# Performance work log

Hardware: AMD Instinct MI355X
Metric: run time of the kernel (lower is better)

## Reference

```python
import jax, jax.numpy as jnp
import numpy as np

HIDDEN = 256
HEADS = 8
HEAD_DIM = HIDDEN // HEADS
N = 4096
EPS = 1e-5


def setup_inputs() -> dict:
    key = jax.random.key(0)
    ks = jax.random.split(key, 16)
    s = HIDDEN ** -0.5
    inp = {
        "A": jax.random.uniform(ks[0], (N, N), dtype=jnp.float32),
        "h": jax.random.normal(ks[1], (N, HIDDEN), dtype=jnp.float32),
        # Linear layers stored torch-style as [out, in]
        "Wq": jax.random.normal(ks[2], (HIDDEN, HIDDEN), jnp.float32) * s,
        "bq": jnp.zeros((HIDDEN,), jnp.float32),
        "Wk": jax.random.normal(ks[3], (HIDDEN, HIDDEN), jnp.float32) * s,
        "bk": jnp.zeros((HIDDEN,), jnp.float32),
        "Wv": jax.random.normal(ks[4], (HIDDEN, HIDDEN), jnp.float32) * s,
        "bv": jnp.zeros((HIDDEN,), jnp.float32),
        "Wo": jax.random.normal(ks[5], (HIDDEN, HIDDEN), jnp.float32) * s,
        "bo": jnp.zeros((HIDDEN,), jnp.float32),
        "W1": jax.random.normal(ks[6], (2 * HIDDEN, HIDDEN), jnp.float32) * s,
        "c1": jnp.zeros((2 * HIDDEN,), jnp.float32),
        "W2": jax.random.normal(ks[7], (HIDDEN, 2 * HIDDEN), jnp.float32) * (2 * HIDDEN) ** -0.5,
        "c2": jnp.zeros((HIDDEN,), jnp.float32),
        "g1": jnp.ones((HIDDEN,), jnp.float32),
        "be1": jnp.zeros((HIDDEN,), jnp.float32),
        "g2": jnp.ones((HIDDEN,), jnp.float32),
        "be2": jnp.zeros((HIDDEN,), jnp.float32),
    }
    return inp


def _batchnorm(x, gamma, beta):
    # BatchNorm1d training mode: biased batch stats over node axis
    mean = x.mean(axis=0)
    var = ((x - mean) ** 2).mean(axis=0)
    return (x - mean) * jax.lax.rsqrt(var + EPS) * gamma + beta


def _mha(A, h, Wq, bq, Wk, bk, Wv, bv, Wo, bo):
    n = h.shape[0]
    scaling = HEAD_DIM ** -0.5
    # NOTE: raw reshape [N, H*d] -> (H, N, d), exactly as the torch code (no transpose)
    q = ((h @ Wq.T + bq).reshape(HEADS, n, HEAD_DIM)) * scaling
    k = (h @ Wk.T + bk).reshape(HEADS, n, HEAD_DIM)
    v = (h @ Wv.T + bv).reshape(HEADS, n, HEAD_DIM)
    t = jnp.einsum('hnd,hmd->hnm', q, k)          # [H, N, N]
    attn = jax.nn.softmax(t * A, axis=2)          # multiplicative adjacency mask
    out = jnp.einsum('hnm,hmd->hnd', attn, v)     # [H, N, d]
    return out.reshape(n, -1) @ Wo.T + bo         # raw reshape back, as in torch


def reference(A, h, Wq, bq, Wk, bk, Wv, bv, Wo, bo, W1, c1, W2, c2, g1, be1, g2, be2):
    h1 = h
    x = _mha(A, h, Wq, bq, Wk, bk, Wv, bv, Wo, bo)
    x = _batchnorm(x + h1, g1, be1)
    h2 = x
    x = jax.nn.relu(x @ W1.T + c1) @ W2.T + c2
    return _batchnorm(h2 + x, g2, be2)
```

## Files before the change

kernel.cpp:

```cpp
#include <hip/hip_runtime.h>

#define N_NODES 4096
#define HID 256
#define NHEADS 8
#define HDIM 32
#define EPSV 1e-5f
#define M2LOG 11.541560327111707f

typedef __bf16 bf16x8 __attribute__((ext_vector_type(8)));
typedef __bf16 bf16x4 __attribute__((ext_vector_type(4)));
typedef float f32x4 __attribute__((ext_vector_type(4)));

__device__ inline float fexp2(float x) {
    float r;
    asm("v_exp_f32 %0, %1" : "=v"(r) : "v"(x));
    return r;
}

__device__ inline uint4 pack8(float4 a, float4 b) {
    bf16x8 p;
    p[0]=(__bf16)a.x; p[1]=(__bf16)a.y; p[2]=(__bf16)a.z; p[3]=(__bf16)a.w;
    p[4]=(__bf16)b.x; p[5]=(__bf16)b.y; p[6]=(__bf16)b.z; p[7]=(__bf16)b.w;
    return __builtin_bit_cast(uint4, p);
}
__device__ inline float4 nmad4(float4 x, float4 s, float4 sh) {
    return make_float4(fmaf(x.x,s.x,sh.x), fmaf(x.y,s.y,sh.y),
                       fmaf(x.z,s.z,sh.z), fmaf(x.w,s.w,sh.w));
}

__launch_bounds__(256)
__global__ void gemm_mfma(const float* __restrict__ X, const float* __restrict__ W,
                          const float* __restrict__ bias, const float* __restrict__ resid,
                          float* __restrict__ C,
                          const float* __restrict__ nscale, const float* __restrict__ nshift,
                          const float* __restrict__ rscale, const float* __restrict__ rshift,
                          int M, int N, int K, float scale, int do_relu) {
    __shared__ uint4 xl[2][512];
    __shared__ uint4 wl[2][512];
    const int bm = blockIdx.x * 64, bn = blockIdx.y * 64;
    const int t = threadIdx.x;
    const int w = t >> 6, l = t & 63, g = l >> 4, nl = l & 15;
    const int srow = t >> 3, seg = t & 7;
    const int sx = (seg & 3) << 1;
    const int d0 = seg*64 + (srow ^ sx);
    const int d1 = seg*64 + ((srow + 32) ^ sx);
    const float* xp = X + (size_t)(bm + srow)*K + seg*8;
    const float* wp = W + (size_t)(bn + srow)*K + seg*8;
    const size_t rstep = (size_t)32*K;

    f32x4 acc[4];
    #pragma unroll
    for (int nf = 0; nf < 4; ++nf) acc[nf] = (f32x4){0.f,0.f,0.f,0.f};

    {
        float4 x0 = *(const float4*)(xp),          x1 = *(const float4*)(xp + 4);
        float4 x2 = *(const float4*)(xp + rstep),  x3 = *(const float4*)(xp + rstep + 4);
        if (nscale) {
            float4 s0 = *(const float4*)(nscale + seg*8), s1 = *(const float4*)(nscale + seg*8 + 4);
            float4 h0 = *(const float4*)(nshift + seg*8), h1 = *(const float4*)(nshift + seg*8 + 4);
            x0 = nmad4(x0,s0,h0); x1 = nmad4(x1,s1,h1);
            x2 = nmad4(x2,s0,h0); x3 = nmad4(x3,s1,h1);
        }
        float4 w0 = *(const float4*)(wp),          w1 = *(const float4*)(wp + 4);
        float4 w2 = *(const float4*)(wp + rstep),  w3 = *(const float4*)(wp + rstep + 4);
        xl[0][d0] = pack8(x0, x1); xl[0][d1] = pack8(x2, x3);
        wl[0][d0] = pack8(w0, w1); wl[0][d1] = pack8(w2, w3);
    }
    __syncthreads();

    for (int k0 = 0; k0 < K; k0 += 64) {
        const int cur = (k0 >> 6) & 1;
        const bool nxt = (k0 + 64) < K;
        float4 nx0, nx1, nx2, nx3, nw0, nw1, nw2, nw3;
        if (nxt) {
            const int kk = k0 + 64;
            nx0 = *(const float4*)(xp + kk);          nx1 = *(const float4*)(xp + kk + 4);
            nx2 = *(const float4*)(xp + rstep + kk);  nx3 = *(const float4*)(xp + rstep + kk + 4);
            if (nscale) {
                float4 s0 = *(const float4*)(nscale + kk + seg*8), s1 = *(const float4*)(nscale + kk + seg*8 + 4);
                float4 h0 = *(const float4*)(nshift + kk + seg*8), h1 = *(const float4*)(nshift + kk + seg*8 + 4);
                nx0 = nmad4(nx0,s0,h0); nx1 = nmad4(nx1,s1,h1);
                nx2 = nmad4(nx2,s0,h0); nx3 = nmad4(nx3,s1,h1);
            }
            nw0 = *(const float4*)(wp + kk);          nw1 = *(const float4*)(wp + kk + 4);
            nw2 = *(const float4*)(wp + rstep + kk);  nw3 = *(const float4*)(wp + rstep + kk + 4);
        }
        __builtin_amdgcn_s_setprio(1);
        #pragma unroll
        for (int ks = 0; ks < 2; ++ks) {
            bf16x8 af = __builtin_bit_cast(bf16x8, xl[cur][(ks*4 + g)*64 + ((w*16 + nl) ^ (g << 1))]);
            #pragma unroll
            for (int nf = 0; nf < 4; ++nf) {
                bf16x8 bfr = __builtin_bit_cast(bf16x8, wl[cur][(ks*4 + g)*64 + ((nf*16 + nl) ^ (g << 1))]);
                acc[nf] = __builtin_amdgcn_mfma_f32_16x16x32_bf16(af, bfr, acc[nf], 0, 0, 0);
            }
        }
        __builtin_amdgcn_s_setprio(0);
        if (nxt) {
            xl[cur^1][d0] = pack8(nx0, nx1); xl[cur^1][d1] = pack8(nx2, nx3);
            wl[cur^1][d0] = pack8(nw0, nw1); wl[cur^1][d1] = pack8(nw2, nw3);
        }
        __syncthreads();
    }

    #pragma unroll
    for (int nf = 0; nf < 4; ++nf) {
        const int col = bn + nf*16 + nl;
        const float bb = bias[col];
        float rs = 1.f, rh = 0.f;
        if (rscale) { rs = rscale[col]; rh = rshift[col]; }
        #pragma unroll
        for (int r = 0; r < 4; ++r) {
            const int row = bm + w*16 + g*4 + r;
            float v = acc[nf][r] + bb;
            if (resid) {
                float rv = resid[(size_t)row*N + col];
                v += rscale ? fmaf(rv, rs, rh) : rv;
            }
            v *= scale;
            if (do_relu) v = fmaxf(v, 0.f);
            C[(size_t)row*N + col] = v;
        }
    }
}

__launch_bounds__(256)
__global__ void gemm_qkv(const float* __restrict__ X,
                         const float* __restrict__ Wq, const float* __restrict__ Wk,
                         const float* __restrict__ Wv, const float* __restrict__ bq,
                         const float* __restrict__ bk, const float* __restrict__ bv,
                         __bf16* __restrict__ qhat, __bf16* __restrict__ khat,
                         __bf16* __restrict__ vhat) {
    const int K = 256;
    __shared__ uint4 xl[2][512];
    __shared__ uint4 wl[2][512];
    const int z = blockIdx.z;
    const float* W = (z == 0) ? Wq : (z == 1) ? Wk : Wv;
    const float* bias = (z == 0) ? bq : (z == 1) ? bk : bv;
    __bf16* hat = (z == 0) ? qhat : (z == 1) ? khat : vhat;
    const float scale = (z == 0) ? 0.25506595325f : 1.f;

    const int bm = blockIdx.x * 64, bn = blockIdx.y * 64;
    const int t = threadIdx.x;
    const int w = t >> 6, l = t & 63, g = l >> 4, nl = l & 15;
    const int srow = t >> 3, seg = t & 7;
    const int sx = (seg & 3) << 1;
    const int d0 = seg*64 + (srow ^ sx);
    const int d1 = seg*64 + ((srow + 32) ^ sx);
    const float* xp = X + (size_t)(bm + srow)*K + seg*8;
    const float* wp = W + (size_t)(bn + srow)*K + seg*8;
    const size_t rstep = (size_t)32*K;

    f32x4 acc[4];
    #pragma unroll
    for (int nf = 0; nf < 4; ++nf) acc[nf] = (f32x4){0.f,0.f,0.f,0.f};

    {
        float4 x0 = *(const float4*)(xp),          x1 = *(const float4*)(xp + 4);
        float4 x2 = *(const float4*)(xp + rstep),  x3 = *(const float4*)(xp + rstep + 4);
        float4 w0 = *(const float4*)(wp),          w1 = *(const float4*)(wp + 4);
        float4 w2 = *(const float4*)(wp + rstep),  w3 = *(const float4*)(wp + rstep + 4);
        xl[0][d0] = pack8(x0, x1); xl[0][d1] = pack8(x2, x3);
        wl[0][d0] = pack8(w0, w1); wl[0][d1] = pack8(w2, w3);
    }
    __syncthreads();

    for (int k0 = 0; k0 < K; k0 += 64) {
        const int cur = (k0 >> 6) & 1;
        const bool nxt = (k0 + 64) < K;
        float4 nx0, nx1, nx2, nx3, nw0, nw1, nw2, nw3;
        if (nxt) {
            nx0 = *(const float4*)(xp + k0 + 64);          nx1 = *(const float4*)(xp + k0 + 68);
            nx2 = *(const float4*)(xp + rstep + k0 + 64);  nx3 = *(const float4*)(xp + rstep + k0 + 68);
            nw0 = *(const float4*)(wp + k0 + 64);          nw1 = *(const float4*)(wp + k0 + 68);
            nw2 = *(const float4*)(wp + rstep + k0 + 64);  nw3 = *(const float4*)(wp + rstep + k0 + 68);
        }
        __builtin_amdgcn_s_setprio(1);
        #pragma unroll
        for (int ks = 0; ks < 2; ++ks) {
            bf16x8 af = __builtin_bit_cast(bf16x8, xl[cur][(ks*4 + g)*64 + ((w*16 + nl) ^ (g << 1))]);
            #pragma unroll
            for (int nf = 0; nf < 4; ++nf) {
                bf16x8 bfr = __builtin_bit_cast(bf16x8, wl[cur][(ks*4 + g)*64 + ((nf*16 + nl) ^ (g << 1))]);
                acc[nf] = __builtin_amdgcn_mfma_f32_16x16x32_bf16(af, bfr, acc[nf], 0, 0, 0);
            }
        }
        __builtin_amdgcn_s_setprio(0);
        if (nxt) {
            xl[cur^1][d0] = pack8(nx0, nx1); xl[cur^1][d1] = pack8(nx2, nx3);
            wl[cur^1][d0] = pack8(nw0, nw1); wl[cur^1][d1] = pack8(nw2, nw3);
        }
        __syncthreads();
    }

    #pragma unroll
    for (int nf = 0; nf < 4; ++nf) {
        const int col = bn + nf*16 + nl;
        const float bb = bias[col];
        #pragma unroll
        for (int r = 0; r < 4; ++r) {
            const int row = bm + w*16 + g*4 + r;
            float v = (acc[nf][r] + bb) * scale;
            const int hh = row >> 9;
            const int nn = ((row & 511) << 3) | (col >> 5);
            hat[((size_t)(hh*4096 + nn))*32 + (col & 31)] = (__bf16)v;
        }
    }
}

__launch_bounds__(256)
__global__ void transpose_vhat(const __bf16* __restrict__ vhat, __bf16* __restrict__ vT) {
    const int h = blockIdx.y, n0 = blockIdx.x * 64;
    __shared__ __bf16 tile[64][40];
    const int t = threadIdx.x;
    {
        int n = t >> 2, dd0 = (t & 3) * 8;
        *(uint4*)&tile[n][dd0] = *(const uint4*)(vhat + ((size_t)(h*4096 + n0 + n))*32 + dd0);
    }
    __syncthreads();
    {
        int d = t >> 3, ns = (t & 7) * 8;
        uint4 ov;
        __bf16* op = (__bf16*)&ov;
        #pragma unroll
        for (int j = 0; j < 8; ++j) op[j] = tile[ns + j][d];
        *(uint4*)(vT + ((size_t)(h*32 + d))*4096 + n0 + ns) = ov;
    }
}

__launch_bounds__(256)
__global__ void attn_mfma(const __bf16* __restrict__ qh, const __bf16* __restrict__ kh,
                          const __bf16* __restrict__ vT, const float* __restrict__ A,
                          float* __restrict__ Opart, float* __restrict__ Lpart, int mlen) {
    __shared__ float A_lds[2][32][76];
    __shared__ uint4 p_lds[4][2][64];

    const int t = threadIdx.x;
    const int w = t >> 6, l = t & 63;
    const int g = l >> 4, nl = l & 15;
    const int h = blockIdx.y * 4 + w;
    const int n0 = blockIdx.x * 32;
    const int z = blockIdx.z;
    const int m_begin = z * mlen;
    const int nsteps = mlen >> 6;

    bf16x8 qf[2];
    #pragma unroll
    for (int nf = 0; nf < 2; ++nf)
        qf[nf] = *(const bf16x8*)(qh + ((size_t)(h*4096 + n0 + nf*16 + nl))*32 + g*8);

    f32x4 oacc[2][2];
    #pragma unroll
    for (int nf = 0; nf < 2; ++nf) {
        oacc[nf][0] = (f32x4){0.f,0.f,0.f,0.f};
        oacc[nf][1] = (f32x4){0.f,0.f,0.f,0.f};
    }
    float Li[2] = {0.f, 0.f};

    const int aq = t >> 3, am = (t & 7) * 8;
    const float* Abase = A + (size_t)(n0 + aq)*N_NODES + m_begin + am;
    const __bf16* kbase = kh + ((size_t)h*4096 + nl)*32 + g*8;
    const __bf16* vbase = vT + ((size_t)h*32 + nl)*4096 + g*8;

    *(float4*)&A_lds[0][aq][am]   = *(const float4*)(Abase);
    *(float4*)&A_lds[0][aq][am+4] = *(const float4*)(Abase + 4);
    bf16x8 kcur[4];
    #pragma unroll
    for (int tt = 0; tt < 4; ++tt)
        kcur[tt] = *(const bf16x8*)(kbase + (size_t)(m_begin + tt*16)*32);
    asm volatile("s_waitcnt lgkmcnt(0)" ::: "memory");
    __builtin_amdgcn_s_barrier();

    for (int s = 0; s < nsteps; ++s) {
        const int cur = s & 1;
        const int m0 = m_begin + s*64;
        const int sn = (s + 1 < nsteps) ? (s + 1) : s;
        const int mn = m_begin + sn*64;

        bf16x8 vcur[4];
        #pragma unroll
        for (int half = 0; half < 2; ++half)
            #pragma unroll
            for (int dt = 0; dt < 2; ++dt)
                vcur[half*2+dt] = *(const bf16x8*)(vbase + (size_t)dt*16*4096 + m0 + half*32);
        float4 a0n = *(const float4*)(Abase + sn*64);
        float4 a1n = *(const float4*)(Abase + sn*64 + 4);
        bf16x8 knx[4];
        #pragma unroll
        for (int tt = 0; tt < 4; ++tt)
            knx[tt] = *(const bf16x8*)(kbase + (size_t)(mn + tt*16)*32);
        __builtin_amdgcn_sched_barrier(0);

        #pragma unroll
        for (int half = 0; half < 2; ++half) {
            #pragma unroll
            for (int tt2 = 0; tt2 < 2; ++tt2) {
                const int tt = half*2 + tt2;
                f32x4 st[2];
                __builtin_amdgcn_s_setprio(1);
                #pragma unroll
                for (int nf = 0; nf < 2; ++nf) {
                    f32x4 zz = (f32x4){0.f,0.f,0.f,0.f};
                    st[nf] = __builtin_amdgcn_mfma_f32_16x16x32_bf16(kcur[tt], qf[nf], zz, 0, 0, 0);
                }
                __builtin_amdgcn_s_setprio(0);
                #pragma unroll
                for (int nf = 0; nf < 2; ++nf) {
                    const f32x4 a4 = *(const f32x4*)&A_lds[cur][nf*16 + nl][tt*16 + g*4];
                    float p0 = fexp2(fmaf(st[nf][0], a4[0], -M2LOG));
                    float p1 = fexp2(fmaf(st[nf][1], a4[1], -M2LOG));
                    float p2 = fexp2(fmaf(st[nf][2], a4[2], -M2LOG));
                    float p3 = fexp2(fmaf(st[nf][3], a4[3], -M2LOG));
                    Li[nf] += (p0 + p1) + (p2 + p3);
                    bf16x4 pk;
                    pk[0] = (__bf16)p0; pk[1] = (__bf16)p1;
                    pk[2] = (__bf16)p2; pk[3] = (__bf16)p3;
                    const int gm = tt2*2 + (g >> 1);
                    *(bf16x4*)((char*)&p_lds[w][nf][0] + (gm*16 + (nl ^ (gm << 1)))*16 + (g & 1)*8) = pk;
                }
            }
            __builtin_amdgcn_s_setprio(1);
            #pragma unroll
            for (int nf = 0; nf < 2; ++nf) {
                bf16x8 pf = __builtin_bit_cast(bf16x8, p_lds[w][nf][g*16 + (nl ^ (g << 1))]);
                #pragma unroll
                for (int dt = 0; dt < 2; ++dt)
                    oacc[nf][dt] = __builtin_amdgcn_mfma_f32_16x16x32_bf16(vcur[half*2+dt], pf, oacc[nf][dt], 0, 0, 0);
            }
            __builtin_amdgcn_s_setprio(0);
        }

        if (s + 1 < nsteps) {
            *(float4*)&A_lds[cur^1][aq][am]   = a0n;
            *(float4*)&A_lds[cur^1][aq][am+4] = a1n;
        }
        #pragma unroll
        for (int tt = 0; tt < 4; ++tt) kcur[tt] = knx[tt];
        asm volatile("s_waitcnt lgkmcnt(0)" ::: "memory");
        __builtin_amdgcn_s_barrier();
    }

    #pragma unroll
    for (int nf = 0; nf < 2; ++nf) {
        Li[nf] += __shfl_xor(Li[nf], 16);
        Li[nf] += __shfl_xor(Li[nf], 32);
        const int nq = n0 + nf*16 + nl;
        float* ob = Opart + ((size_t)(z*NHEADS + h)*4096 + nq)*32;
        #pragma unroll
        for (int dt = 0; dt < 2; ++dt)
            *(float4*)(ob + dt*16 + g*4) = make_float4(oacc[nf][dt][0], oacc[nf][dt][1],
                                                       oacc[nf][dt][2], oacc[nf][dt][3]);
        if (g == 0)
            Lpart[(z*NHEADS + h)*4096 + nq] = Li[nf];
    }
}

__launch_bounds__(256)
__global__ void attn_combine(const float* __restrict__ Opart, const float* __restrict__ Lpart,
                             float* __restrict__ AO, int nsplit) {
    const int idx4 = (blockIdx.x * 256 + threadIdx.x) * 4;
    const int hn = idx4 >> 5;
    float L = 0.f;
    float4 acc = make_float4(0.f, 0.f, 0.f, 0.f);
    for (int zz = 0; zz < nsplit; ++zz) {
        L += Lpart[zz*32768 + hn];
        float4 o = *(const float4*)(Opart + (size_t)zz*1048576 + idx4);
        acc.x += o.x; acc.y += o.y; acc.z += o.z; acc.w += o.w;
    }
    const float inv = 1.f / L;
    *(float4*)(AO + idx4) = make_float4(acc.x*inv, acc.y*inv, acc.z*inv, acc.w*inv);
}

__launch_bounds__(256)
__global__ void colstats_part(const float* __restrict__ X, float* __restrict__ ps,
                              float* __restrict__ pq) {
    const int b = blockIdx.x, t = threadIdx.x;
    float s = 0.f, q = 0.f;
    const float* p = X + (size_t)b*64*HID + t;
    #pragma unroll 8
    for (int r = 0; r < 64; ++r) {
        float v = p[r*HID];
        s += v; q = fmaf(v, v, q);
    }
    ps[b*HID + t] = s;
    pq[b*HID + t] = q;
}

__launch_bounds__(256)
__global__ void colstats_fin(const float* __restrict__ ps, const float* __restrict__ pq,
                             const float* __restrict__ gam, const float* __restrict__ bet,
                             float* __restrict__ scl, float* __restrict__ shf) {
    const int c = threadIdx.x;
    float s = 0.f, q = 0.f;
    #pragma unroll 8
    for (int b = 0; b < 64; ++b) { s += ps[b*HID + c]; q += pq[b*HID + c]; }
    const float m = s * (1.f/4096.f);
    const float rstd = rsqrtf(q*(1.f/4096.f) - m*m + EPSV);
    const float sc = rstd * gam[c];
    scl[c] = sc;
    shf[c] = fmaf(-m, sc, bet[c]);
}

__launch_bounds__(256)
__global__ void bnorm_apply4(const float* __restrict__ X, const float* __restrict__ scl,
                             const float* __restrict__ shf, float* __restrict__ Y) {
    const int base = (blockIdx.x * 256 + threadIdx.x) * 4;
    const int c = base & (HID - 1);
    float4 x = *(const float4*)(X + base);
    float4 o;
    o.x = fmaf(x.x, scl[c+0], shf[c+0]);
    o.y = fmaf(x.y, scl[c+1], shf[c+1]);
    o.z = fmaf(x.z, scl[c+2], shf[c+2]);
    o.w = fmaf(x.w, scl[c+3], shf[c+3]);
    *(float4*)(Y + base) = o;
}

extern "C" void kernel_launch(void* const* d_in, const int* in_sizes, int n_in,
                              void* d_out, int out_size, void* d_ws, size_t ws_size,
                              hipStream_t stream) {
    const float* A  = (const float*)d_in[0];
    const float* h  = (const float*)d_in[1];
    const float* Wq = (const float*)d_in[2];
    const float* bq = (const float*)d_in[3];
    const float* Wk = (const float*)d_in[4];
    const float* bk = (const float*)d_in[5];
    const float* Wv = (const float*)d_in[6];
    const float* bv = (const float*)d_in[7];
    const float* Wo = (const float*)d_in[8];
    const float* bo = (const float*)d_in[9];
    const float* W1 = (const float*)d_in[10];
    const float* c1 = (const float*)d_in[11];
    const float* W2 = (const float*)d_in[12];
    const float* c2 = (const float*)d_in[13];
    const float* g1 = (const float*)d_in[14];
    const float* be1= (const float*)d_in[15];
    const float* g2 = (const float*)d_in[16];
    const float* be2= (const float*)d_in[17];

    char* wsb = (char*)d_ws;
    const size_t MiB = (size_t)1 << 20;
    const int nsplit = (ws_size >= 43*MiB) ? 8 : (ws_size >= 26*MiB) ? 4 : 2;
    const int mlen = N_NODES / nsplit;

    __bf16* qhat = (__bf16*)(wsb + 0*MiB);
    __bf16* khat = (__bf16*)(wsb + 2*MiB);
    __bf16* vhat = (__bf16*)(wsb + 4*MiB);
    __bf16* vT   = (__bf16*)(wsb + 6*MiB);
    float* Opart = (float*)(wsb + 8*MiB);
    float* Lpart = (float*)(wsb + 8*MiB + (size_t)nsplit*4*MiB);
    char* statb  = wsb + 8*MiB + (size_t)nsplit*4*MiB + 1*MiB;
    float* partS = (float*)statb;
    float* partQ = partS + 64*HID;
    float* scale1 = partQ + 64*HID;
    float* shift1 = scale1 + HID;
    float* scale2 = shift1 + HID;
    float* shift2 = scale2 + HID;
    float* AO = (float*)(wsb + 0*MiB);
    float* Y1 = (float*)(wsb + 4*MiB);
    float* F1 = (float*)(wsb + 8*MiB);
    float* Y2 = (float*)(wsb + 0*MiB);

    gemm_qkv<<<dim3(64, 4, 3), 256, 0, stream>>>(h, Wq, Wk, Wv, bq, bk, bv, qhat, khat, vhat);
    transpose_vhat<<<dim3(64, 8), 256, 0, stream>>>(vhat, vT);

    attn_mfma<<<dim3(128, 2, nsplit), 256, 0, stream>>>(qhat, khat, vT, A, Opart, Lpart, mlen);
    attn_combine<<<1024, 256, 0, stream>>>(Opart, Lpart, AO, nsplit);

    gemm_mfma<<<dim3(64, 4), 256, 0, stream>>>(AO, Wo, bo, h, Y1,
                                               nullptr, nullptr, nullptr, nullptr,
                                               4096, 256, 256, 1.f, 0);

    colstats_part<<<64, 256, 0, stream>>>(Y1, partS, partQ);
    colstats_fin<<<1, 256, 0, stream>>>(partS, partQ, g1, be1, scale1, shift1);

    gemm_mfma<<<dim3(64, 8), 256, 0, stream>>>(Y1, W1, c1, nullptr, F1,
                                               scale1, shift1, nullptr, nullptr,
                                               4096, 512, 256, 1.f, 1);
    gemm_mfma<<<dim3(64, 4), 256, 0, stream>>>(F1, W2, c2, Y1, Y2,
                                               nullptr, nullptr, scale1, shift1,
                                               4096, 256, 512, 1.f, 0);

    colstats_part<<<64, 256, 0, stream>>>(Y2, partS, partQ);
    colstats_fin<<<1, 256, 0, stream>>>(partS, partQ, g2, be2, scale2, shift2);
    bnorm_apply4<<<1024, 256, 0, stream>>>(Y2, scale2, shift2, (float*)d_out);
}
```

Baseline: 139.4 us.

## Double attention block size to 64 queries with 512 threads and unrolled K ping-pong

Each attention block now covers 64 query rows with 8 waves (4 heads x 2 query halves) instead of 32 rows with 4 waves. Each A tile staged in LDS is therefore shared by twice as many waves, and the grid is halved. The main loop is also unrolled by two, alternating between two K register buffers so the per-step copy of next-step K into current-step K goes away. The trade-off is more LDS and more registers per block, plus a larger barrier group, which may reduce occupancy. The two-step unroll also assumes nsteps is even.

```diff
diff --git a/kernel.cpp b/kernel.cpp
--- a/kernel.cpp
+++ b/kernel.cpp
@@ -228,18 +228,20 @@
     }
 }
 
-__launch_bounds__(256)
-__global__ void attn_mfma(const __bf16* __restrict__ qh, const __bf16* __restrict__ kh,
+__launch_bounds__(512, 2)
+__global__ void attn_mfma(const __bf16* __restrict__ qh_, const __bf16* __restrict__ kh,
                           const __bf16* __restrict__ vT, const float* __restrict__ A,
                           float* __restrict__ Opart, float* __restrict__ Lpart, int mlen) {
-    __shared__ float A_lds[2][32][76];
-    __shared__ uint4 p_lds[4][2][64];
+    __shared__ float A_lds[2][64][68];
+    __shared__ uint4 p_lds[8][2][64];
 
     const int t = threadIdx.x;
     const int w = t >> 6, l = t & 63;
     const int g = l >> 4, nl = l & 15;
-    const int h = blockIdx.y * 4 + w;
-    const int n0 = blockIdx.x * 32;
+    const int hh = w & 3, qhf = w >> 2;
+    const int h = blockIdx.y * 4 + hh;
+    const int n0 = blockIdx.x * 64;
+    const int qbase = n0 + qhf*32;
     const int z = blockIdx.z;
     const int m_begin = z * mlen;
     const int nsteps = mlen >> 6;
@@ -247,7 +249,7 @@
     bf16x8 qf[2];
     #pragma unroll
     for (int nf = 0; nf < 2; ++nf)
-        qf[nf] = *(const bf16x8*)(qh + ((size_t)(h*4096 + n0 + nf*16 + nl))*32 + g*8);
+        qf[nf] = *(const bf16x8*)(qh_ + ((size_t)(h*4096 + qbase + nf*16 + nl))*32 + g*8);
 
     f32x4 oacc[2][2];
     #pragma unroll
@@ -264,87 +266,88 @@
 
     *(float4*)&A_lds[0][aq][am]   = *(const float4*)(Abase);
     *(float4*)&A_lds[0][aq][am+4] = *(const float4*)(Abase + 4);
-    bf16x8 kcur[4];
+    bf16x8 ka[4], kb[4];
     #pragma unroll
     for (int tt = 0; tt < 4; ++tt)
-        kcur[tt] = *(const bf16x8*)(kbase + (size_t)(m_begin + tt*16)*32);
+        ka[tt] = *(const bf16x8*)(kbase + (size_t)(m_begin + tt*16)*32);
     asm volatile("s_waitcnt lgkmcnt(0)" ::: "memory");
     __builtin_amdgcn_s_barrier();
 
-    for (int s = 0; s < nsteps; ++s) {
-        const int cur = s & 1;
-        const int m0 = m_begin + s*64;
-        const int sn = (s + 1 < nsteps) ? (s + 1) : s;
-        const int mn = m_begin + sn*64;
-
-        bf16x8 vcur[4];
-        #pragma unroll
-        for (int half = 0; half < 2; ++half)
-            #pragma unroll
-            for (int dt = 0; dt < 2; ++dt)
-                vcur[half*2+dt] = *(const bf16x8*)(vbase + (size_t)dt*16*4096 + m0 + half*32);
-        float4 a0n = *(const float4*)(Abase + sn*64);
-        float4 a1n = *(const float4*)(Abase + sn*64 + 4);
-        bf16x8 knx[4];
-        #pragma unroll
-        for (int tt = 0; tt < 4; ++tt)
-            knx[tt] = *(const bf16x8*)(kbase + (size_t)(mn + tt*16)*32);
-        __builtin_amdgcn_sched_barrier(0);
-
-        #pragma unroll
-        for (int half = 0; half < 2; ++half) {
-            #pragma unroll
-            for (int tt2 = 0; tt2 < 2; ++tt2) {
-                const int tt = half*2 + tt2;
-                f32x4 st[2];
-                __builtin_amdgcn_s_setprio(1);
-                #pragma unroll
-                for (int nf = 0; nf < 2; ++nf) {
-                    f32x4 zz = (f32x4){0.f,0.f,0.f,0.f};
-                    st[nf] = __builtin_amdgcn_mfma_f32_16x16x32_bf16(kcur[tt], qf[nf], zz, 0, 0, 0);
-                }
-                __builtin_amdgcn_s_setprio(0);
-                #pragma unroll
-                for (int nf = 0; nf < 2; ++nf) {
-                    const f32x4 a4 = *(const f32x4*)&A_lds[cur][nf*16 + nl][tt*16 + g*4];
-                    float p0 = fexp2(fmaf(st[nf][0], a4[0], -M2LOG));
-                    float p1 = fexp2(fmaf(st[nf][1], a4[1], -M2LOG));
-                    float p2 = fexp2(fmaf(st[nf][2], a4[2], -M2LOG));
-                    float p3 = fexp2(fmaf(st[nf][3], a4[3], -M2LOG));
-                    Li[nf] += (p0 + p1) + (p2 + p3);
-                    bf16x4 pk;
-                    pk[0] = (__bf16)p0; pk[1] = (__bf16)p1;
-                    pk[2] = (__bf16)p2; pk[3] = (__bf16)p3;
-                    const int gm = tt2*2 + (g >> 1);
-                    *(bf16x4*)((char*)&p_lds[w][nf][0] + (gm*16 + (nl ^ (gm << 1)))*16 + (g & 1)*8) = pk;
-                }
-            }
-            __builtin_amdgcn_s_setprio(1);
-            #pragma unroll
-            for (int nf = 0; nf < 2; ++nf) {
-                bf16x8 pf = __builtin_bit_cast(bf16x8, p_lds[w][nf][g*16 + (nl ^ (g << 1))]);
-                #pragma unroll
-                for (int dt = 0; dt < 2; ++dt)
-                    oacc[nf][dt] = __builtin_amdgcn_mfma_f32_16x16x32_bf16(vcur[half*2+dt], pf, oacc[nf][dt], 0, 0, 0);
-            }
-            __builtin_amdgcn_s_setprio(0);
-        }
-
-        if (s + 1 < nsteps) {
-            *(float4*)&A_lds[cur^1][aq][am]   = a0n;
-            *(float4*)&A_lds[cur^1][aq][am+4] = a1n;
-        }
-        #pragma unroll
-        for (int tt = 0; tt < 4; ++tt) kcur[tt] = knx[tt];
-        asm volatile("s_waitcnt lgkmcnt(0)" ::: "memory");
-        __builtin_amdgcn_s_barrier();
-    }
+#define ATTN_STEP(S, KUSE, KPRE)                                                      \
+    {                                                                                 \
+        const int cur = (S) & 1;                                                      \
+        const int m0 = m_begin + (S)*64;                                              \
+        const int sn = ((S) + 1 < nsteps) ? (S) + 1 : (S);                            \
+        const int mn = m_begin + sn*64;                                               \
+        bf16x8 vcur[4];                                                               \
+        _Pragma("unroll")                                                             \
+        for (int half = 0; half < 2; ++half)                                          \
+            _Pragma("unroll")                                                         \
+            for (int dt = 0; dt < 2; ++dt)                                            \
+                vcur[half*2+dt] = *(const bf16x8*)(vbase + (size_t)dt*16*4096 + m0 + half*32); \
+        float4 a0n = *(const float4*)(Abase + sn*64);                                 \
+        float4 a1n = *(const float4*)(Abase + sn*64 + 4);                             \
+        _Pragma("unroll")                                                             \
+        for (int tt = 0; tt < 4; ++tt)                                                \
+            KPRE[tt] = *(const bf16x8*)(kbase + (size_t)(mn + tt*16)*32);             \
+        __builtin_amdgcn_sched_barrier(0);                                            \
+        _Pragma("unroll")                                                             \
+        for (int half = 0; half < 2; ++half) {                                        \
+            _Pragma("unroll")                                                         \
+            for (int tt2 = 0; tt2 < 2; ++tt2) {                                       \
+                const int tt = half*2 + tt2;                                          \
+                f32x4 st[2];                                                          \
+                __builtin_amdgcn_s_setprio(1);                                        \
+                _Pragma("unroll")                                                     \
+                for (int nf = 0; nf < 2; ++nf) {                                      \
+                    f32x4 zz = (f32x4){0.f,0.f,0.f,0.f};                              \
+                    st[nf] = __builtin_amdgcn_mfma_f32_16x16x32_bf16(KUSE[tt], qf[nf], zz, 0, 0, 0); \
+                }                                                                     \
+                __builtin_amdgcn_s_setprio(0);                                        \
+                _Pragma("unroll")                                                     \
+                for (int nf = 0; nf < 2; ++nf) {                                      \
+                    const f32x4 a4 = *(const f32x4*)&A_lds[cur][qhf*32 + nf*16 + nl][tt*16 + g*4]; \
+                    float p0 = fexp2(fmaf(st[nf][0], a4[0], -M2LOG));                 \
+                    float p1 = fexp2(fmaf(st[nf][1], a4[1], -M2LOG));                 \
+                    float p2 = fexp2(fmaf(st[nf][2], a4[2], -M2LOG));                 \
+                    float p3 = fexp2(fmaf(st[nf][3], a4[3], -M2LOG));                 \
+                    Li[nf] += (p0 + p1) + (p2 + p3);                                  \
+                    bf16x4 pk;                                                        \
+                    pk[0] = (__bf16)p0; pk[1] = (__bf16)p1;                           \
+                    pk[2] = (__bf16)p2; pk[3] = (__bf16)p3;                           \
+                    const int gm = tt2*2 + (g >> 1);                                  \
+                    *(bf16x4*)((char*)&p_lds[w][nf][0] + (gm*16 + (nl ^ (gm << 1)))*16 + (g & 1)*8) = pk; \
+                }                                                                     \
+            }                                                                         \
+            __builtin_amdgcn_s_setprio(1);                                            \
+            _Pragma("unroll")                                                         \
+            for (int nf = 0; nf < 2; ++nf) {                                          \
+                bf16x8 pf = __builtin_bit_cast(bf16x8, p_lds[w][nf][g*16 + (nl ^ (g << 1))]); \
+                _Pragma("unroll")                                                     \
+                for (int dt = 0; dt < 2; ++dt)                                        \
+                    oacc[nf][dt] = __builtin_amdgcn_mfma_f32_16x16x32_bf16(vcur[half*2+dt], pf, oacc[nf][dt], 0, 0, 0); \
+            }                                                                         \
+            __builtin_amdgcn_s_setprio(0);                                            \
+        }                                                                             \
+        if (sn != (S)) {                                                              \
+            *(float4*)&A_lds[cur^1][aq][am]   = a0n;                                  \
+            *(float4*)&A_lds[cur^1][aq][am+4] = a1n;                                  \
+        }                                                                             \
+        asm volatile("s_waitcnt lgkmcnt(0)" ::: "memory");                            \
+        __builtin_amdgcn_s_barrier();                                                 \
+    }
+
+    for (int s = 0; s < nsteps; s += 2) {
+        ATTN_STEP(s,     ka, kb);
+        ATTN_STEP(s + 1, kb, ka);
+    }
+#undef ATTN_STEP
 
     #pragma unroll
     for (int nf = 0; nf < 2; ++nf) {
         Li[nf] += __shfl_xor(Li[nf], 16);
         Li[nf] += __shfl_xor(Li[nf], 32);
-        const int nq = n0 + nf*16 + nl;
+        const int nq = qbase + nf*16 + nl;
         float* ob = Opart + ((size_t)(z*NHEADS + h)*4096 + nq)*32;
         #pragma unroll
         for (int dt = 0; dt < 2; ++dt)
@@ -463,7 +466,7 @@
     gemm_qkv<<<dim3(64, 4, 3), 256, 0, stream>>>(h, Wq, Wk, Wv, bq, bk, bv, qhat, khat, vhat);
     transpose_vhat<<<dim3(64, 8), 256, 0, stream>>>(vhat, vT);
 
-    attn_mfma<<<dim3(128, 2, nsplit), 256, 0, stream>>>(qhat, khat, vT, A, Opart, Lpart, mlen);
+    attn_mfma<<<dim3(64, 2, nsplit), 512, 0, stream>>>(qhat, khat, vT, A, Opart, Lpart, mlen);
     attn_combine<<<1024, 256, 0, stream>>>(Opart, Lpart, AO, nsplit);
 
     gemm_mfma<<<dim3(64, 4), 256, 0, stream>>>(AO, Wo, bo, h, Y1,
```

Result: slower. 152.8 us (+9.7%).
